# Kernel tuning notes

Measured on AMD Instinct MI355X. Metric: run time of the kernel, lower is better.

Reference implementation:

```python
import jax, jax.numpy as jnp
import numpy as np
from jax import lax

EPS = 1e-8
ROUTINGS = 3


def squash(u, axis=-1):
    norm = jnp.linalg.norm(u, axis=axis, keepdims=True)
    scale = norm ** 2 / (1 + norm ** 2) / (norm + EPS)
    return scale * u


def conv2d(x, w, b, stride):
    y = lax.conv_general_dilated(x, w, window_strides=(stride, stride), padding='VALID',
                                 dimension_numbers=('NCHW', 'OIHW', 'NCHW'))
    return y + b[None, :, None, None]


def setup_inputs() -> dict:
    key = jax.random.key(0)
    ks = jax.random.split(key, 6)
    x = jax.random.normal(ks[0], (512, 1, 28, 28), dtype=jnp.float32)
    conv1_w = 0.1 * jax.random.normal(ks[1], (256, 1, 9, 9), dtype=jnp.float32)
    conv1_b = 0.1 * jax.random.normal(ks[2], (256,), dtype=jnp.float32)
    pc_w = 0.01 * jax.random.normal(ks[3], (256, 256, 9, 9), dtype=jnp.float32)
    pc_b = 0.01 * jax.random.normal(ks[4], (256,), dtype=jnp.float32)
    caps_w = 0.01 * jax.random.normal(ks[5], (10, 1152, 16, 8), dtype=jnp.float32)
    return {"x": x, "conv1_w": conv1_w, "conv1_b": conv1_b,
            "pc_w": pc_w, "pc_b": pc_b, "caps_w": caps_w}


def reference(x, conv1_w, conv1_b, pc_w, pc_b, caps_w):
    B = x.shape[0]
    # conv1 + relu: [B,1,28,28] -> [B,256,20,20]
    h = jax.nn.relu(conv2d(x, conv1_w, conv1_b, stride=1))
    # primary capsules: [B,256,20,20] -> [B,256,6,6] -> [B,1152,8], squash
    h = conv2d(h, pc_w, pc_b, stride=2)
    u = squash(h.reshape(B, 1152, 8))
    # votes: weight [O,I,Do,Di] x u [B,I,Di] -> x_hat [B,O,I,Do]
    x_hat = jnp.einsum('oidk,bik->boid', caps_w, u)
    x_hat_det = lax.stop_gradient(x_hat)
    b_logits = jnp.zeros((B, caps_w.shape[0], caps_w.shape[1]), dtype=x_hat.dtype)
    out_caps = None
    for i in range(ROUTINGS):
        c = jax.nn.softmax(b_logits, axis=1)  # softmax over output caps
        if i == ROUTINGS - 1:
            out_caps = squash(jnp.sum(c[..., None] * x_hat, axis=2))  # [B,O,Do]
        else:
            v = squash(jnp.sum(c[..., None] * x_hat_det, axis=2))  # [B,O,Do]
            b_logits = b_logits + jnp.einsum('bod,boid->boi', v, x_hat_det)
    length = jnp.linalg.norm(out_caps, axis=-1)  # [B,O]
    return length
```

## Files before the change

### kernel.cpp

```cpp
#include <hip/hip_runtime.h>
#include <hip/hip_bf16.h>
#include <hip/hip_fp16.h>
#include <math.h>

#define EPS 1e-8f

typedef __attribute__((ext_vector_type(8))) short bf16x8;
typedef __attribute__((ext_vector_type(8))) _Float16 f16x8;
typedef __attribute__((ext_vector_type(4))) float f32x4;

__device__ static inline unsigned short f2bf(float f) {
    __hip_bfloat16 h = __float2bfloat16(f);
    return *reinterpret_cast<unsigned short*>(&h);
}
__device__ static inline unsigned short f2h(float f) {
    __half h = __float2half(f);
    return *reinterpret_cast<unsigned short*>(&h);
}

__device__ static inline void gld_lds16(const void* g, void* l) {
    __builtin_amdgcn_global_load_lds((const __attribute__((address_space(1))) void*)g,
                                     (__attribute__((address_space(3))) void*)l, 16, 0, 0);
}

__device__ static inline void h8tof(uint4 w, float* f) {
    float2 a = __half22float2(*(__half2*)&w.x);
    float2 b = __half22float2(*(__half2*)&w.y);
    float2 c = __half22float2(*(__half2*)&w.z);
    float2 d = __half22float2(*(__half2*)&w.w);
    f[0] = a.x; f[1] = a.y; f[2] = b.x; f[3] = b.y;
    f[4] = c.x; f[5] = c.y; f[6] = d.x; f[7] = d.y;
}

__global__ void k_prep(const float* __restrict__ x, unsigned short* __restrict__ xh,
                       const float* __restrict__ w1, unsigned short* __restrict__ wt1h,
                       const float* __restrict__ cw, __half* __restrict__ cwh) {
    int idx = blockIdx.x * 256 + threadIdx.x;
    if (idx < 401408) {
        xh[idx] = f2h(x[idx]);
    } else if (idx < 401408 + 24576) {
        int j = idx - 401408;
        int n = j / 96, k = j % 96;
        wt1h[j] = (k < 81) ? f2h(w1[n * 81 + k]) : (unsigned short)0;
    } else {
        int j = idx - 401408 - 24576;
        cwh[j] = __float2half(cw[j]);
    }
}

__global__ void k_tw2(const float* __restrict__ pw, unsigned short* __restrict__ wt2t) {
    int idx = blockIdx.x * 256 + threadIdx.x;
    int oc = idx / 20736, k = idx % 20736;
    int q = k >> 8, ic = k & 255;
    wt2t[idx] = f2bf(pw[oc * 20736 + ic * 81 + q]);
}

__global__ __launch_bounds__(256) void k_conv1(const unsigned short* __restrict__ xh,
                                               const unsigned short* __restrict__ wt1h,
                                               const float* __restrict__ b1,
                                               unsigned short* __restrict__ h1) {
    __shared__ unsigned short Asm[128 * 104];
    __shared__ unsigned short Bsm[128 * 104];
    const int tid = threadIdx.x;
    const int wave = tid >> 6, lane = tid & 63;
    const int ln15 = lane & 15, quad = lane >> 4;
    const int m0 = blockIdx.x * 128;
    const int n0 = blockIdx.y * 128;
    const int wm = (wave >> 1) * 64, wn = (wave & 1) * 64;

    for (int c = tid; c < 1536; c += 256) {
        int r = c / 12, ch = c % 12;
        uint4 v = *(const uint4*)(wt1h + (size_t)(n0 + r) * 96 + ch * 8);
        *(uint4*)(&Bsm[r * 104 + ch * 8]) = v;
    }
    for (int s = 0; s < 5; ++s) {
        int id = s * 256 + tid;
        if (id < 1152) {
            int m_l = id & 127, kh = id >> 7;
            int m = m0 + m_l;
            int b = m / 400, sp = m % 400;
            int oh = sp / 20, ow = sp % 20;
            const unsigned short* src = xh + b * 784 + (oh + kh) * 28 + ow;
            unsigned short* drow = &Asm[m_l * 104 + kh * 9];
#pragma unroll
            for (int w = 0; w < 9; ++w) drow[w] = src[w];
        }
    }
    for (int z = tid; z < 1920; z += 256) {
        int r = z / 15, kk = 81 + z % 15;
        Asm[r * 104 + kk] = 0;
    }
    __syncthreads();

    f32x4 acc[4][4];
#pragma unroll
    for (int i = 0; i < 4; ++i)
#pragma unroll
        for (int j = 0; j < 4; ++j) acc[i][j] = (f32x4)(0.f);

#pragma unroll
    for (int ks = 0; ks < 3; ++ks) {
        int k0 = (ks * 4 + quad) * 8;
        f16x8 af[4], bfr[4];
#pragma unroll
        for (int i = 0; i < 4; ++i)
            af[i] = *(const f16x8*)&Asm[(wm + i * 16 + ln15) * 104 + k0];
#pragma unroll
        for (int j = 0; j < 4; ++j)
            bfr[j] = *(const f16x8*)&Bsm[(wn + j * 16 + ln15) * 104 + k0];
#pragma unroll
        for (int i = 0; i < 4; ++i)
#pragma unroll
            for (int j = 0; j < 4; ++j)
                acc[i][j] = __builtin_amdgcn_mfma_f32_16x16x32_f16(
                    af[i], bfr[j], acc[i][j], 0, 0, 0);
    }

    float bias[4];
#pragma unroll
    for (int j = 0; j < 4; ++j) bias[j] = b1[n0 + wn + j * 16 + ln15];
#pragma unroll
    for (int i = 0; i < 4; ++i) {
#pragma unroll
        for (int r = 0; r < 4; ++r) {
            int m = m0 + wm + i * 16 + quad * 4 + r;
            unsigned short* dst = h1 + (size_t)m * 256 + n0 + wn;
#pragma unroll
            for (int j = 0; j < 4; ++j) {
                float v = acc[i][j][r] + bias[j];
                dst[j * 16 + ln15] = f2bf(v > 0.f ? v : 0.f);
            }
        }
    }
}

__global__ __launch_bounds__(256) void k_conv2(const unsigned short* __restrict__ h1,
                                               const unsigned short* __restrict__ wt2t,
                                               float* __restrict__ h2a) {
    __shared__ short Asm[128 * 64];
    __shared__ short Bsm[128 * 64];

    const int tid  = threadIdx.x;
    const int wave = tid >> 6, lane = tid & 63;
    const int ln15 = lane & 15, quad = lane >> 4, ln7 = lane & 7;
    const int nz = blockIdx.x;
    const int n0 = (nz >> 2) * 128;
    const int zz = nz & 3;
    const int m0 = blockIdx.y * 128;
    const int kt0 = zz * 81;
    const int wm = (wave >> 1) * 64, wn = (wave & 1) * 64;

    const int rbase = wave * 32 + (lane >> 3);
    const int cswz8 = ((lane & 7) ^ ((lane >> 3) & 7)) * 8;

    size_t aptr[4];
    size_t bptr[4];
#pragma unroll
    for (int s = 0; s < 4; ++s) {
        int r = rbase + s * 8;
        int m = m0 + r;
        int b = m / 36, sp = m % 36;
        int oh = sp / 6, ow = sp % 6;
        aptr[s] = (size_t)((b * 20 + 2 * oh) * 20 + 2 * ow) * 256 + cswz8;
        bptr[s] = (size_t)(n0 + r) * 20736 + cswz8;
    }
    short* alds = &Asm[(wave * 32) * 64 + lane * 8];
    short* blds = &Bsm[(wave * 32) * 64 + lane * 8];

    f32x4 acc[4][4];
#pragma unroll
    for (int i = 0; i < 4; ++i)
#pragma unroll
        for (int j = 0; j < 4; ++j) acc[i][j] = (f32x4)(0.f);

    int q0 = kt0 >> 2;
    int kh = q0 / 9, kw = q0 - kh * 9;
    int pix = (kh * 20 + kw) * 256;

    for (int kt = kt0; kt < kt0 + 81; ++kt) {
        size_t aoff = (size_t)pix + ((kt & 3) << 6);
        size_t boff = (size_t)kt << 6;
#pragma unroll
        for (int s = 0; s < 4; ++s)
            gld_lds16(h1 + aptr[s] + aoff, alds + s * 512);
#pragma unroll
        for (int s = 0; s < 4; ++s)
            gld_lds16(wt2t + bptr[s] + boff, blds + s * 512);
        __syncthreads();
#pragma unroll
        for (int ks = 0; ks < 2; ++ks) {
            bf16x8 af[4], bfr[4];
#pragma unroll
            for (int i = 0; i < 4; ++i) {
                int chunk = ((ks << 2) + quad) ^ ln7;
                af[i] = *(const bf16x8*)&Asm[(wm + i * 16 + ln15) * 64 + chunk * 8];
            }
#pragma unroll
            for (int j = 0; j < 4; ++j) {
                int chunk = ((ks << 2) + quad) ^ ln7;
                bfr[j] = *(const bf16x8*)&Bsm[(wn + j * 16 + ln15) * 64 + chunk * 8];
            }
#pragma unroll
            for (int i = 0; i < 4; ++i)
#pragma unroll
                for (int j = 0; j < 4; ++j)
                    acc[i][j] = __builtin_amdgcn_mfma_f32_16x16x32_bf16(
                        af[i], bfr[j], acc[i][j], 0, 0, 0);
        }
        __syncthreads();
        if ((kt & 3) == 3) {
            if (kw == 8) { kw = 0; ++kh; pix += 12 * 256; }
            else         { ++kw;       pix += 256; }
        }
    }

    float* zs = h2a + (size_t)zz * 4718592;
#pragma unroll
    for (int i = 0; i < 4; ++i) {
#pragma unroll
        for (int r = 0; r < 4; ++r) {
            int m = m0 + wm + i * 16 + quad * 4 + r;
            float* dst = zs + (size_t)m * 256 + n0 + wn;
#pragma unroll
            for (int j = 0; j < 4; ++j)
                dst[j * 16 + ln15] = acc[i][j][r];
        }
    }
}

__global__ __launch_bounds__(256) void k_squash(const float* __restrict__ h2a,
                                                const float* __restrict__ pb,
                                                unsigned short* __restrict__ u) {
    __shared__ float tile[36 * 260];
    const int tid = threadIdx.x;
    const int b = blockIdx.x;
    const float* base = h2a + (size_t)b * 36 * 256;
    for (int idx = tid; idx < 9216; idx += 256) {
        int sp = idx >> 8, c = idx & 255;
        float v = pb[c];
#pragma unroll
        for (int z = 0; z < 4; ++z) v += base[(size_t)z * 4718592 + sp * 256 + c];
        tile[sp * 260 + c] = v;
    }
    __syncthreads();
    for (int i2 = tid; i2 < 1152; i2 += 256) {
        int f0 = i2 * 8;
        float val[8];
        float n2 = 0.f;
#pragma unroll
        for (int e = 0; e < 8; ++e) {
            int f = f0 + e;
            int c = f / 36, sp = f - c * 36;
            val[e] = tile[sp * 260 + c];
            n2 += val[e] * val[e];
        }
        float n = sqrtf(n2);
        float s = n2 / (1.f + n2) / (n + EPS);
        unsigned short o8[8];
#pragma unroll
        for (int e = 0; e < 8; ++e) o8[e] = f2h(val[e] * s);
        *(uint4*)(u + (size_t)b * 9216 + f0) = *(uint4*)o8;
    }
}

__global__ __launch_bounds__(256) void k_xhat(const unsigned short* __restrict__ u,
                                              const __half* __restrict__ cwh,
                                              __half* __restrict__ xhat,
                                              float* __restrict__ s0) {
    __shared__ float ush[9216];
    __shared__ float part[4][16];
    const int b = blockIdx.x;
    const int t = threadIdx.x;
    const int wave = t >> 6;
    {
        const uint4* src = (const uint4*)(u + (size_t)b * 9216);
        for (int idx = t; idx < 1152; idx += 256) {
            uint4 v = src[idx];
            h8tof(v, &ush[idx * 8]);
        }
    }
    __syncthreads();

    for (int o = 0; o < 10; ++o) {
        float s_loc[16];
#pragma unroll
        for (int d = 0; d < 16; ++d) s_loc[d] = 0.f;
        for (int i = t; i < 1152; i += 256) {
            float ui[8];
            *(float4*)ui       = *(const float4*)&ush[i * 8];
            *(float4*)(ui + 4) = *(const float4*)&ush[i * 8 + 4];
            const uint4* wp = (const uint4*)(cwh + ((size_t)(o * 1152 + i) << 7));
            unsigned short xv[16];
#pragma unroll
            for (int d = 0; d < 16; ++d) {
                float f[8];
                h8tof(wp[d], f);
                float xh = f[0] * ui[0] + f[1] * ui[1] + f[2] * ui[2] + f[3] * ui[3]
                         + f[4] * ui[4] + f[5] * ui[5] + f[6] * ui[6] + f[7] * ui[7];
                s_loc[d] += xh;
                xv[d] = f2h(xh);
            }
            __half* dst = xhat + ((size_t)((b * 10 + o) * 1152 + i)) * 16;
            *(uint4*)dst       = *(uint4*)xv;
            *(uint4*)(dst + 8) = *(uint4*)(xv + 8);
        }
#pragma unroll
        for (int off = 32; off > 0; off >>= 1)
#pragma unroll
            for (int d = 0; d < 16; ++d) s_loc[d] += __shfl_down(s_loc[d], off, 64);
        if ((t & 63) == 0) {
#pragma unroll
            for (int d = 0; d < 16; ++d) part[wave][d] = s_loc[d];
        }
        __syncthreads();
        if (t < 16)
            s0[(b * 10 + o) * 16 + t] = part[0][t] + part[1][t] + part[2][t] + part[3][t];
        __syncthreads();
    }
}

__global__ __launch_bounds__(640) void k_routing(const __half* __restrict__ xhat,
                                                 const float* __restrict__ s0,
                                                 float* __restrict__ out) {
    __shared__ float dots[10][1152];
    __shared__ float sv[10][16];
    __shared__ float vsum[10][16];
    __shared__ float scale_sh[10];
    const int t = threadIdx.x;
    const int b = blockIdx.x;
    const int o = t >> 6, lane = t & 63;
    const __half* xb = xhat + ((size_t)(b * 10 + o) * 1152) * 16;

    if (t < 160) {
        int oo = t >> 4, d = t & 15;
        sv[oo][d] = 0.1f * s0[(b * 10 + oo) * 16 + d];
    }
    __syncthreads();
    if (t < 10) {
        float n2 = 0.f;
#pragma unroll
        for (int d = 0; d < 16; ++d) n2 += sv[t][d] * sv[t][d];
        float n = sqrtf(n2);
        scale_sh[t] = n2 / (1.f + n2) / (n + EPS);
    }
    __syncthreads();
    if (t < 160) vsum[t >> 4][t & 15] = sv[t >> 4][t & 15] * scale_sh[t >> 4];
    __syncthreads();

    for (int pass = 1; pass <= 2; ++pass) {
        float vs[16];
#pragma unroll
        for (int d = 0; d < 16; ++d) vs[d] = vsum[o][d];
        float s_loc[16];
#pragma unroll
        for (int d = 0; d < 16; ++d) s_loc[d] = 0.f;

        for (int g = 0; g < 6; ++g) {
            uint4 xq[3][2];
#pragma unroll
            for (int j = 0; j < 3; ++j) {
                int i = g * 192 + j * 64 + lane;
                const uint4* p = (const uint4*)(xb + (size_t)i * 16);
                xq[j][0] = p[0];
                xq[j][1] = p[1];
                float f0[8], f1[8];
                h8tof(xq[j][0], f0);
                h8tof(xq[j][1], f1);
                float dd = 0.f;
#pragma unroll
                for (int d = 0; d < 8; ++d) dd += vs[d] * f0[d] + vs[d + 8] * f1[d];
                dots[o][i] = dd;
            }
            __syncthreads();
            if (t < 192) {
                int i = g * 192 + t;
                float dv[10];
#pragma unroll
                for (int oo = 0; oo < 10; ++oo) dv[oo] = dots[oo][i];
                float mx = dv[0];
#pragma unroll
                for (int oo = 1; oo < 10; ++oo) mx = fmaxf(mx, dv[oo]);
                float se = 0.f;
#pragma unroll
                for (int oo = 0; oo < 10; ++oo) { dv[oo] = __expf(dv[oo] - mx); se += dv[oo]; }
                float si = 1.f / se;
#pragma unroll
                for (int oo = 0; oo < 10; ++oo) dots[oo][i] = dv[oo] * si;
            }
            __syncthreads();
#pragma unroll
            for (int j = 0; j < 3; ++j) {
                int i = g * 192 + j * 64 + lane;
                float c = dots[o][i];
                float f0[8], f1[8];
                h8tof(xq[j][0], f0);
                h8tof(xq[j][1], f1);
#pragma unroll
                for (int d = 0; d < 8; ++d) {
                    s_loc[d]     += c * f0[d];
                    s_loc[d + 8] += c * f1[d];
                }
            }
        }
#pragma unroll
        for (int off = 32; off > 0; off >>= 1)
#pragma unroll
            for (int d = 0; d < 16; ++d) s_loc[d] += __shfl_down(s_loc[d], off, 64);
        if (lane == 0) {
#pragma unroll
            for (int d = 0; d < 16; ++d) sv[o][d] = s_loc[d];
        }
        __syncthreads();
        if (pass == 1) {
            if (t < 10) {
                float n2 = 0.f;
#pragma unroll
                for (int d = 0; d < 16; ++d) n2 += sv[t][d] * sv[t][d];
                float n = sqrtf(n2);
                scale_sh[t] = n2 / (1.f + n2) / (n + EPS);
            }
            __syncthreads();
            if (t < 160) {
                int oo = t >> 4, d = t & 15;
                vsum[oo][d] += sv[oo][d] * scale_sh[oo];
            }
            __syncthreads();
        } else {
            if (t < 10) {
                float n2 = 0.f;
#pragma unroll
                for (int d = 0; d < 16; ++d) n2 += sv[t][d] * sv[t][d];
                float n = sqrtf(n2);
                out[b * 10 + t] = (n2 / (1.f + n2)) * (n / (n + EPS));
            }
        }
    }
}

extern "C" void kernel_launch(void* const* d_in, const int* in_sizes, int n_in,
                              void* d_out, int out_size, void* d_ws, size_t ws_size,
                              hipStream_t stream) {
    const float* x  = (const float*)d_in[0];
    const float* w1 = (const float*)d_in[1];
    const float* b1 = (const float*)d_in[2];
    const float* pw = (const float*)d_in[3];
    const float* pb = (const float*)d_in[4];
    const float* cw = (const float*)d_in[5];
    float* out = (float*)d_out;

    char* ws = (char*)d_ws;
    unsigned short* h1   = (unsigned short*)ws;
    float*          h2a  = (float*)(ws + 104857600);
    unsigned short* wt2t = (unsigned short*)(ws + 180355072);
    __half*         xhat = (__half*)ws;
    unsigned short* u    = (unsigned short*)(ws + 190971904);
    __half*         cwh  = (__half*)(ws + 200409088);
    unsigned short* xh16 = (unsigned short*)(ws + 203358208);
    unsigned short* wt1h = (unsigned short*)(ws + 204161024);
    float*          s0   = (float*)(ws + 204210176);

    k_prep<<<7424, 256, 0, stream>>>(x, xh16, w1, wt1h, cw, cwh);
    k_tw2<<<20736, 256, 0, stream>>>(pw, wt2t);
    k_conv1<<<dim3(1600, 2), 256, 0, stream>>>(xh16, wt1h, b1, h1);
    k_conv2<<<dim3(8, 144), 256, 0, stream>>>(h1, wt2t, h2a);
    k_squash<<<512, 256, 0, stream>>>(h2a, pb, u);
    k_xhat<<<512, 256, 0, stream>>>(u, cwh, xhat, s0);
    k_routing<<<512, 640, 0, stream>>>(xhat, s0, out);
}
```

Before: 740.0 us.

## Use 32x32x16 MFMA in conv2 with 6-way split-K and M-major grid

The primary-capsule conv GEMM switches from 16x16x32 to 32x32x16 bf16 MFMA tiles, so each wave issues fewer, larger MFMAs and does fewer LDS fragment reads. Split-K goes from 4 to 6 slices, giving 1728 blocks instead of 1152 for better CU fill. The grid is reordered so blocks sharing a weight tile run together. The cost is 50% more fp32 partial-sum traffic for squash to read and reduce, plus a larger workspace with shifted buffer offsets.

```diff
diff --git a/kernel.cpp b/kernel.cpp
--- a/kernel.cpp
+++ b/kernel.cpp
@@ -8,6 +8,7 @@
 typedef __attribute__((ext_vector_type(8))) short bf16x8;
 typedef __attribute__((ext_vector_type(8))) _Float16 f16x8;
 typedef __attribute__((ext_vector_type(4))) float f32x4;
+typedef __attribute__((ext_vector_type(16))) float f32x16;
 
 __device__ static inline unsigned short f2bf(float f) {
     __hip_bfloat16 h = __float2bfloat16(f);
@@ -142,12 +143,11 @@
 
     const int tid  = threadIdx.x;
     const int wave = tid >> 6, lane = tid & 63;
-    const int ln15 = lane & 15, quad = lane >> 4, ln7 = lane & 7;
-    const int nz = blockIdx.x;
-    const int n0 = (nz >> 2) * 128;
-    const int zz = nz & 3;
-    const int m0 = blockIdx.y * 128;
-    const int kt0 = zz * 81;
+    const int ln31 = lane & 31, ln7 = lane & 7, khalf = lane >> 5;
+    const int m0 = blockIdx.x * 128;
+    const int n0 = blockIdx.y * 128;
+    const int zz = blockIdx.z;
+    const int kt0 = zz * 54;
     const int wm = (wave >> 1) * 64, wn = (wave & 1) * 64;
 
     const int rbase = wave * 32 + (lane >> 3);
@@ -167,17 +167,17 @@
     short* alds = &Asm[(wave * 32) * 64 + lane * 8];
     short* blds = &Bsm[(wave * 32) * 64 + lane * 8];
 
-    f32x4 acc[4][4];
-#pragma unroll
-    for (int i = 0; i < 4; ++i)
-#pragma unroll
-        for (int j = 0; j < 4; ++j) acc[i][j] = (f32x4)(0.f);
+    f32x16 acc[2][2];
+#pragma unroll
+    for (int i = 0; i < 2; ++i)
+#pragma unroll
+        for (int j = 0; j < 2; ++j) acc[i][j] = (f32x16)(0.f);
 
     int q0 = kt0 >> 2;
     int kh = q0 / 9, kw = q0 - kh * 9;
     int pix = (kh * 20 + kw) * 256;
 
-    for (int kt = kt0; kt < kt0 + 81; ++kt) {
+    for (int kt = kt0; kt < kt0 + 54; ++kt) {
         size_t aoff = (size_t)pix + ((kt & 3) << 6);
         size_t boff = (size_t)kt << 6;
 #pragma unroll
@@ -188,23 +188,20 @@
             gld_lds16(wt2t + bptr[s] + boff, blds + s * 512);
         __syncthreads();
 #pragma unroll
-        for (int ks = 0; ks < 2; ++ks) {
-            bf16x8 af[4], bfr[4];
-#pragma unroll
-            for (int i = 0; i < 4; ++i) {
-                int chunk = ((ks << 2) + quad) ^ ln7;
-                af[i] = *(const bf16x8*)&Asm[(wm + i * 16 + ln15) * 64 + chunk * 8];
-            }
-#pragma unroll
-            for (int j = 0; j < 4; ++j) {
-                int chunk = ((ks << 2) + quad) ^ ln7;
-                bfr[j] = *(const bf16x8*)&Bsm[(wn + j * 16 + ln15) * 64 + chunk * 8];
-            }
-#pragma unroll
-            for (int i = 0; i < 4; ++i)
-#pragma unroll
-                for (int j = 0; j < 4; ++j)
-                    acc[i][j] = __builtin_amdgcn_mfma_f32_16x16x32_bf16(
+        for (int ks = 0; ks < 4; ++ks) {
+            int slot = ((ks << 1) + khalf) ^ ln7;
+            bf16x8 af[2], bfr[2];
+#pragma unroll
+            for (int i = 0; i < 2; ++i)
+                af[i] = *(const bf16x8*)&Asm[(wm + i * 32 + ln31) * 64 + slot * 8];
+#pragma unroll
+            for (int j = 0; j < 2; ++j)
+                bfr[j] = *(const bf16x8*)&Bsm[(wn + j * 32 + ln31) * 64 + slot * 8];
+#pragma unroll
+            for (int i = 0; i < 2; ++i)
+#pragma unroll
+                for (int j = 0; j < 2; ++j)
+                    acc[i][j] = __builtin_amdgcn_mfma_f32_32x32x16_bf16(
                         af[i], bfr[j], acc[i][j], 0, 0, 0);
         }
         __syncthreads();
@@ -216,14 +213,15 @@
 
     float* zs = h2a + (size_t)zz * 4718592;
 #pragma unroll
-    for (int i = 0; i < 4; ++i) {
-#pragma unroll
-        for (int r = 0; r < 4; ++r) {
-            int m = m0 + wm + i * 16 + quad * 4 + r;
-            float* dst = zs + (size_t)m * 256 + n0 + wn;
-#pragma unroll
-            for (int j = 0; j < 4; ++j)
-                dst[j * 16 + ln15] = acc[i][j][r];
+    for (int i = 0; i < 2; ++i) {
+#pragma unroll
+        for (int j = 0; j < 2; ++j) {
+#pragma unroll
+            for (int reg = 0; reg < 16; ++reg) {
+                int row = (reg & 3) + 8 * (reg >> 2) + 4 * khalf;
+                int m = m0 + wm + i * 32 + row;
+                zs[(size_t)m * 256 + n0 + wn + j * 32 + ln31] = acc[i][j][reg];
+            }
         }
     }
 }
@@ -239,7 +237,7 @@
         int sp = idx >> 8, c = idx & 255;
         float v = pb[c];
 #pragma unroll
-        for (int z = 0; z < 4; ++z) v += base[(size_t)z * 4718592 + sp * 256 + c];
+        for (int z = 0; z < 6; ++z) v += base[(size_t)z * 4718592 + sp * 256 + c];
         tile[sp * 260 + c] = v;
     }
     __syncthreads();
@@ -451,18 +449,18 @@
     char* ws = (char*)d_ws;
     unsigned short* h1   = (unsigned short*)ws;
     float*          h2a  = (float*)(ws + 104857600);
-    unsigned short* wt2t = (unsigned short*)(ws + 180355072);
+    unsigned short* wt2t = (unsigned short*)(ws + 218103808);
     __half*         xhat = (__half*)ws;
-    unsigned short* u    = (unsigned short*)(ws + 190971904);
-    __half*         cwh  = (__half*)(ws + 200409088);
-    unsigned short* xh16 = (unsigned short*)(ws + 203358208);
-    unsigned short* wt1h = (unsigned short*)(ws + 204161024);
-    float*          s0   = (float*)(ws + 204210176);
+    unsigned short* u    = (unsigned short*)(ws + 228720640);
+    __half*         cwh  = (__half*)(ws + 238157824);
+    unsigned short* xh16 = (unsigned short*)(ws + 241106944);
+    unsigned short* wt1h = (unsigned short*)(ws + 241909760);
+    float*          s0   = (float*)(ws + 241958912);
 
     k_prep<<<7424, 256, 0, stream>>>(x, xh16, w1, wt1h, cw, cwh);
     k_tw2<<<20736, 256, 0, stream>>>(pw, wt2t);
     k_conv1<<<dim3(1600, 2), 256, 0, stream>>>(xh16, wt1h, b1, h1);
-    k_conv2<<<dim3(8, 144), 256, 0, stream>>>(h1, wt2t, h2a);
+    k_conv2<<<dim3(144, 2, 6), 256, 0, stream>>>(h1, wt2t, h2a);
     k_squash<<<512, 256, 0, stream>>>(h2a, pb, u);
     k_xhat<<<512, 256, 0, stream>>>(u, cwh, xhat, s0);
     k_routing<<<512, 640, 0, stream>>>(xhat, s0, out);
```

After: 658.2 us. 11.1% less time.
